# Optimization experiments

Measured on AMD Instinct MI355X. Metric: run time of the kernel, lower is better.

## Reference

```python
import jax, jax.numpy as jnp
import numpy as np

B, S, D, H, DFF, K = 16, 1024, 1024, 16, 4096, 3


def setup_inputs() -> dict:
    key = jax.random.key(0)
    ks = jax.random.split(key, 8)
    f = lambda k, sh: jax.random.normal(k, sh, jnp.float32) * 0.02
    return dict(
        x=jax.random.normal(ks[0], (B, S, D), jnp.float32),
        mask=jnp.ones((B, 1, S), jnp.int32),
        alpha1=jnp.ones((D,), jnp.float32), bias1=jnp.zeros((D,), jnp.float32),
        alpha2=jnp.ones((D,), jnp.float32), bias2=jnp.zeros((D,), jnp.float32),
        W_l1=f(ks[1], (D, 2 * D)), b_l1=jnp.zeros((2 * D,), jnp.float32),
        conv_w=f(ks[2], (H, K)),
        W_l2=f(ks[3], (D, D)), b_l2=jnp.zeros((D,), jnp.float32),
        W_ff1=f(ks[4], (D, DFF)), b_ff1=jnp.zeros((DFF,), jnp.float32),
        W_ff2=f(ks[5], (DFF, D)), b_ff2=jnp.zeros((D,), jnp.float32),
    )


def _norm(x, alpha, bias, eps=1e-6):
    # Norm: alpha * (x - mean) / (std + eps) + bias, torch std is unbiased (ddof=1)
    mu = x.mean(-1, keepdims=True)
    sd = x.std(-1, keepdims=True, ddof=1)
    return alpha * (x - mu) / (sd + eps) + bias


def _lightconv(x, conv_w):
    # x: [B, S, C]; conv_w: [H, K] softmax-normalized over K; channels in a head share kernel
    C = x.shape[-1]
    w = jax.nn.softmax(conv_w, axis=-1)              # [H, K]
    wk = jnp.repeat(w, C // H, axis=0)[:, None, :]   # [C, 1, K] depthwise kernel
    y = jax.lax.conv_general_dilated(
        x.transpose(0, 2, 1), wk, (1,), [(K // 2, (K - 1) // 2)],
        dimension_numbers=('NCH', 'OIH', 'NCH'), feature_group_count=C)
    return y.transpose(0, 2, 1)


def reference(x, mask, alpha1, bias1, alpha2, bias2, W_l1, b_l1, conv_w,
              W_l2, b_l2, W_ff1, b_ff1, W_ff2, b_ff2):
    # --- lightweight-conv sublayer ---
    res = x
    h = _norm(x, alpha1, bias1)
    h = h @ W_l1 + b_l1                         # [B,S,2C]
    a, b = jnp.split(h, 2, axis=-1)
    h = a * jax.nn.sigmoid(b)                   # GLU -> [B,S,C]
    cm = mask[:, -1, :][:, :, None]             # [B,S,1]
    h = jnp.where(cm == 0, 0.0, h)
    h = _lightconv(h, conv_w)
    h = h @ W_l2 + b_l2
    x = res + h
    # --- FFN sublayer ---
    res = x
    h = _norm(x, alpha2, bias2)
    h = jax.nn.relu(h @ W_ff1 + b_ff1) @ W_ff2 + b_ff2
    return res + h
```

## Files before the change

### kernel.cpp

```cpp
#include <hip/hip_runtime.h>

typedef unsigned short ushort_t;
typedef __attribute__((ext_vector_type(8))) short s8v;
typedef __attribute__((ext_vector_type(4))) float f4v;

__device__ __forceinline__ float b2f(ushort_t h) {
    union { unsigned u; float f; } c; c.u = ((unsigned)h) << 16; return c.f;
}
__device__ __forceinline__ ushort_t f2b(float f) {
    union { float f; unsigned u; } c; c.f = f;
    unsigned u = c.u;
    return (ushort_t)((u + 0x7fffu + ((u >> 16) & 1u)) >> 16);
}

__device__ __forceinline__ void glds16(const void* g, void* l) {
    __builtin_amdgcn_global_load_lds(
        (const __attribute__((address_space(1))) void*)g,
        (__attribute__((address_space(3))) void*)l, 16, 0, 0);
}

__global__ __launch_bounds__(256) void trans_k(const float* __restrict__ W,
                                               ushort_t* __restrict__ Wt,
                                               int K, int N) {
    __shared__ float tile[64][65];
    int k0 = blockIdx.x * 64, n0 = blockIdx.y * 64;
    int t = threadIdx.x;
    int c = t & 63, r4 = t >> 6;
#pragma unroll
    for (int i = 0; i < 16; ++i) {
        int r = i * 4 + r4;
        tile[r][c] = W[(size_t)(k0 + r) * N + n0 + c];
    }
    __syncthreads();
#pragma unroll
    for (int i = 0; i < 16; ++i) {
        int r = i * 4 + r4;
        Wt[(size_t)(n0 + r) * K + k0 + c] = f2b(tile[c][r]);
    }
}

__global__ __launch_bounds__(256) void norm_k(const float* __restrict__ x,
                                              const float* __restrict__ al,
                                              const float* __restrict__ be,
                                              ushort_t* __restrict__ out) {
    int row = blockIdx.x;
    const float4* xr = (const float4*)(x + (size_t)row * 1024);
    float4 v = xr[threadIdx.x];
    float s = v.x + v.y + v.z + v.w;
    float q = v.x * v.x + v.y * v.y + v.z * v.z + v.w * v.w;
#pragma unroll
    for (int o = 32; o > 0; o >>= 1) {
        s += __shfl_down(s, o);
        q += __shfl_down(q, o);
    }
    __shared__ float ss[4], qq[4];
    int lane = threadIdx.x & 63, wv = threadIdx.x >> 6;
    if (lane == 0) { ss[wv] = s; qq[wv] = q; }
    __syncthreads();
    s = ss[0] + ss[1] + ss[2] + ss[3];
    q = qq[0] + qq[1] + qq[2] + qq[3];
    float mu = s * (1.f / 1024.f);
    float var = (q - 1024.f * mu * mu) * (1.f / 1023.f);
    var = fmaxf(var, 0.f);
    float inv = 1.f / (sqrtf(var) + 1e-6f);
    float4 a4 = ((const float4*)al)[threadIdx.x];
    float4 b4 = ((const float4*)be)[threadIdx.x];
    ushort4 o4;
    o4.x = f2b(a4.x * (v.x - mu) * inv + b4.x);
    o4.y = f2b(a4.y * (v.y - mu) * inv + b4.y);
    o4.z = f2b(a4.z * (v.z - mu) * inv + b4.z);
    o4.w = f2b(a4.w * (v.w - mu) * inv + b4.w);
    ((ushort4*)(out + (size_t)row * 1024))[threadIdx.x] = o4;
}

__global__ __launch_bounds__(256) void glu_k(const ushort_t* __restrict__ t1,
                                             const int* __restrict__ mask,
                                             ushort_t* __restrict__ g) {
    int i = blockIdx.x * 256 + threadIdx.x;
    int row = i >> 7;
    int cc = (i & 127) << 3;
    int b = row >> 10, s = row & 1023;
    size_t base = (size_t)row * 2048;
    s8v va = *(const s8v*)(t1 + base + cc);
    s8v vb = *(const s8v*)(t1 + base + 1024 + cc);
    float mval = (mask[b * 1024 + s] == 0) ? 0.f : 1.f;
    s8v ov;
#pragma unroll
    for (int j = 0; j < 8; ++j) {
        float a = b2f((ushort_t)va[j]);
        float xx = b2f((ushort_t)vb[j]);
        float sg = 1.f / (1.f + __expf(-xx));
        ov[j] = (short)f2b(a * sg * mval);
    }
    *(s8v*)(g + (size_t)row * 1024 + cc) = ov;
}

__global__ __launch_bounds__(256) void conv_k(const ushort_t* __restrict__ g,
                                              const float* __restrict__ cw,
                                              ushort_t* __restrict__ out) {
    int i = blockIdx.x * 256 + threadIdx.x;
    int row = i >> 7;
    int cc = (i & 127) << 3;
    int s = row & 1023;
    int head = cc >> 6;
    float w0 = cw[head * 3 + 0], w1 = cw[head * 3 + 1], w2 = cw[head * 3 + 2];
    float mx = fmaxf(w0, fmaxf(w1, w2));
    float e0 = __expf(w0 - mx), e1 = __expf(w1 - mx), e2 = __expf(w2 - mx);
    float inv = 1.f / (e0 + e1 + e2);
    w0 = e0 * inv; w1 = e1 * inv; w2 = e2 * inv;
    size_t base = (size_t)row * 1024 + cc;
    s8v z = {0, 0, 0, 0, 0, 0, 0, 0};
    s8v vm = (s > 0)    ? *(const s8v*)(g + base - 1024) : z;
    s8v v0 = *(const s8v*)(g + base);
    s8v vp = (s < 1023) ? *(const s8v*)(g + base + 1024) : z;
    s8v ov;
#pragma unroll
    for (int j = 0; j < 8; ++j) {
        float r = w0 * b2f((ushort_t)vm[j]) + w1 * b2f((ushort_t)v0[j]) +
                  w2 * b2f((ushort_t)vp[j]);
        ov[j] = (short)f2b(r);
    }
    *(s8v*)(out + base) = ov;
}

template <int EPI>
__global__ __launch_bounds__(512, 1) void gemm_k(const ushort_t* __restrict__ A,
                                                 const ushort_t* __restrict__ Bt,
                                                 const float* __restrict__ bias,
                                                 const float* res, float* outf,
                                                 ushort_t* outb, int N, int K) {
    __shared__ char smem[131072] __attribute__((aligned(128)));
    const int NBN = N >> 8;
    const int nwg = gridDim.x;
    const int per = nwg >> 3;
    const int tt = (blockIdx.x & 7) * per + (blockIdx.x >> 3);
    const int gw = NBN << 3;
    const int g = tt / gw;
    const int rem = tt - g * gw;
    const int bm = (g << 3) + (rem & 7);
    const int bn = rem >> 3;

    const int t = threadIdx.x;
    const int l = t & 63, w = t >> 6;
    const int wm = w >> 2, wn = w & 3;
    const int lr = l & 15, lk = l >> 4;

    const int swzel = (((t & 3) ^ ((t >> 3) & 3)) << 3);
    const int r0 = t >> 2;
    const ushort_t* pA0 = A + (size_t)(bm * 256 + r0) * K + swzel;
    const ushort_t* pA1 = pA0 + (size_t)128 * K;
    const ushort_t* pB0 = Bt + (size_t)(bn * 256 + r0) * K + swzel;
    const ushort_t* pB1 = pB0 + (size_t)128 * K;

    const int fswz = ((lk ^ ((lr >> 1) & 3)) << 4);
    int aoff[8], boff[4];
#pragma unroll
    for (int m = 0; m < 8; ++m)
        aoff[m] = (wm * 128 + m * 16 + lr) * 64 + fswz;
#pragma unroll
    for (int n = 0; n < 4; ++n)
        boff[n] = 16384 + (wn * 64 + n * 16 + lr) * 64 + fswz;

    f4v acc[8][4];
#pragma unroll
    for (int m = 0; m < 8; ++m)
#pragma unroll
        for (int n = 0; n < 4; ++n) acc[m][n] = f4v{0.f, 0.f, 0.f, 0.f};

    const int NK = K >> 5;

#pragma unroll
    for (int p = 0; p < 3; ++p) {
        char* d = smem + p * 32768 + t * 16;
        glds16(pA0 + p * 32, d);
        glds16(pA1 + p * 32, d + 8192);
        glds16(pB0 + p * 32, d + 16384);
        glds16(pB1 + p * 32, d + 24576);
    }
    asm volatile("s_waitcnt vmcnt(8)");
    __builtin_amdgcn_s_barrier();
    __builtin_amdgcn_sched_barrier(0);

    s8v aL0[4], bF0[4], aL1[4], bF1[4], aH[4];
#pragma unroll
    for (int m = 0; m < 4; ++m) aL0[m] = *(const s8v*)(smem + aoff[m]);
#pragma unroll
    for (int n = 0; n < 4; ++n) bF0[n] = *(const s8v*)(smem + boff[n]);

#define KSTEP(I, CAL, CBF, NAL, NBF)                                           \
    {                                                                          \
        const int i_ = (I);                                                    \
        const char* cb_ = smem + (size_t)(i_ & 3) * 32768;                     \
        const char* nb_ = smem + (size_t)((i_ + 1) & 3) * 32768;               \
        int st_ = i_ + 3; if (st_ >= NK) st_ = NK - 1;                         \
        char* sd_ = smem + (size_t)((i_ + 3) & 3) * 32768 + t * 16;            \
        const int ko_ = st_ * 32;                                              \
                 \
        _Pragma("unroll")                                                      \
        for (int m = 0; m < 4; ++m) aH[m] = *(const s8v*)(cb_ + aoff[4 + m]);  \
        glds16(pA0 + ko_, sd_);                                                \
        glds16(pA1 + ko_, sd_ + 8192);                                         \
        glds16(pB0 + ko_, sd_ + 16384);                                        \
        glds16(pB1 + ko_, sd_ + 24576);                                        \
        __builtin_amdgcn_s_setprio(1);                                         \
        _Pragma("unroll")                                                      \
        for (int m = 0; m < 4; ++m)                                            \
            _Pragma("unroll")                                                  \
            for (int n = 0; n < 4; ++n)                                        \
                acc[m][n] = __builtin_amdgcn_mfma_f32_16x16x32_bf16(           \
                    CAL[m], CBF[n], acc[m][n], 0, 0, 0);                       \
        __builtin_amdgcn_s_setprio(0);                                         \
        __builtin_amdgcn_sched_barrier(0);                                     \
        asm volatile("s_waitcnt vmcnt(6)");               \
        __builtin_amdgcn_s_barrier();                                          \
        __builtin_amdgcn_sched_barrier(0);                                     \
           \
        _Pragma("unroll")                                                      \
        for (int m = 0; m < 4; ++m) NAL[m] = *(const s8v*)(nb_ + aoff[m]);     \
        _Pragma("unroll")                                                      \
        for (int n = 0; n < 4; ++n) NBF[n] = *(const s8v*)(nb_ + boff[n]);     \
        __builtin_amdgcn_s_setprio(1);                                         \
        _Pragma("unroll")                                                      \
        for (int m = 0; m < 4; ++m)                                            \
            _Pragma("unroll")                                                  \
            for (int n = 0; n < 4; ++n)                                        \
                acc[4 + m][n] = __builtin_amdgcn_mfma_f32_16x16x32_bf16(       \
                    aH[m], CBF[n], acc[4 + m][n], 0, 0, 0);                    \
        __builtin_amdgcn_s_setprio(0);                                         \
    }

    for (int ii = 0; ii < NK; ii += 2) {
        KSTEP(ii, aL0, bF0, aL1, bF1);
        KSTEP(ii + 1, aL1, bF1, aL0, bF0);
    }
#undef KSTEP

    if (EPI == 1) {
#pragma unroll
        for (int n = 0; n < 4; ++n) {
            int gcol = bn * 256 + wn * 64 + n * 16 + lr;
            float bb = bias[gcol];
#pragma unroll
            for (int m = 0; m < 8; ++m) {
#pragma unroll
                for (int r = 0; r < 4; ++r) {
                    int grow = bm * 256 + wm * 128 + m * 16 + lk * 4 + r;
                    size_t oi = (size_t)grow * N + gcol;
                    outf[oi] = acc[m][n][r] + bb + res[oi];
                }
            }
        }
    } else {
        asm volatile("s_waitcnt vmcnt(0)" ::: "memory");
        __builtin_amdgcn_s_barrier();
        float bb4[4];
#pragma unroll
        for (int n = 0; n < 4; ++n)
            bb4[n] = bias[bn * 256 + wn * 64 + n * 16 + lr];
#pragma unroll
        for (int m = 0; m < 8; ++m)
#pragma unroll
            for (int n = 0; n < 4; ++n)
#pragma unroll
                for (int r = 0; r < 4; ++r) {
                    int row = wm * 128 + m * 16 + lk * 4 + r;
                    int colb = ((wn * 64 + n * 16 + lr) * 2) ^ ((row & 3) << 4);
                    float v = acc[m][n][r] + bb4[n];
                    if (EPI == 2) v = fmaxf(v, 0.f);
                    *(ushort_t*)(smem + row * 512 + colb) = f2b(v);
                }
        __builtin_amdgcn_s_barrier();
#pragma unroll
        for (int s = 0; s < 16; ++s) {
            int row = s * 16 + (t >> 5);
            int byt = row * 512 + (((t & 31) * 16) ^ ((row & 3) << 4));
            int grow = bm * 256 + row;
            int gcol = bn * 256 + (t & 31) * 8;
            *(s8v*)(outb + (size_t)grow * N + gcol) = *(const s8v*)(smem + byt);
        }
    }
}

extern "C" void kernel_launch(void* const* d_in, const int* in_sizes, int n_in,
                              void* d_out, int out_size, void* d_ws, size_t ws_size,
                              hipStream_t stream) {
    const float* x      = (const float*)d_in[0];
    const int*   mask   = (const int*)d_in[1];
    const float* alpha1 = (const float*)d_in[2];
    const float* bias1  = (const float*)d_in[3];
    const float* alpha2 = (const float*)d_in[4];
    const float* bias2  = (const float*)d_in[5];
    const float* W_l1   = (const float*)d_in[6];
    const float* b_l1   = (const float*)d_in[7];
    const float* conv_w = (const float*)d_in[8];
    const float* W_l2   = (const float*)d_in[9];
    const float* b_l2   = (const float*)d_in[10];
    const float* W_ff1  = (const float*)d_in[11];
    const float* b_ff1  = (const float*)d_in[12];
    const float* W_ff2  = (const float*)d_in[13];
    const float* b_ff2  = (const float*)d_in[14];
    float* out = (float*)d_out;

    char* ws = (char*)d_ws;
    size_t off = 0;
    auto alloc = [&](size_t b) {
        char* p = ws + off;
        off += (b + 255) & ~(size_t)255;
        return p;
    };
    ushort_t* Wl1t  = (ushort_t*)alloc(2048ull * 1024 * 2);
    ushort_t* Wl2t  = (ushort_t*)alloc(1024ull * 1024 * 2);
    ushort_t* Wff1t = (ushort_t*)alloc(4096ull * 1024 * 2);
    ushort_t* Wff2t = (ushort_t*)alloc(1024ull * 4096 * 2);
    char* regA = alloc(134217728ull);
    ushort_t* B1 = (ushort_t*)alloc(33554432ull);
    ushort_t* C1 = (ushort_t*)alloc(33554432ull);
    ushort_t* t1 = (ushort_t*)regA;
    ushort_t* f1 = (ushort_t*)regA;

    const int R = 16384;

    trans_k<<<dim3(16, 32), 256, 0, stream>>>(W_l1, Wl1t, 1024, 2048);
    trans_k<<<dim3(16, 16), 256, 0, stream>>>(W_l2, Wl2t, 1024, 1024);
    trans_k<<<dim3(16, 64), 256, 0, stream>>>(W_ff1, Wff1t, 1024, 4096);
    trans_k<<<dim3(64, 16), 256, 0, stream>>>(W_ff2, Wff2t, 4096, 1024);

    norm_k<<<R, 256, 0, stream>>>(x, alpha1, bias1, B1);
    gemm_k<0><<<64 * 8, 512, 0, stream>>>(B1, Wl1t, b_l1, nullptr, nullptr, t1, 2048, 1024);
    glu_k<<<8192, 256, 0, stream>>>(t1, mask, B1);
    conv_k<<<8192, 256, 0, stream>>>(B1, conv_w, C1);
    gemm_k<1><<<64 * 4, 512, 0, stream>>>(C1, Wl2t, b_l2, x, out, nullptr, 1024, 1024);

    norm_k<<<R, 256, 0, stream>>>(out, alpha2, bias2, B1);
    gemm_k<2><<<64 * 16, 512, 0, stream>>>(B1, Wff1t, b_ff1, nullptr, nullptr, f1, 4096, 1024);
    gemm_k<1><<<64 * 4, 512, 0, stream>>>(f1, Wff2t, b_ff2, out, out, nullptr, 1024, 4096);
}
```

Baseline: 585.2 us.

## Fuse GLU into conv kernel and switch GEMM to double-buffered 64-wide K steps

```diff
diff --git a/kernel.cpp b/kernel.cpp
--- a/kernel.cpp
+++ b/kernel.cpp
@@ -73,54 +73,41 @@
     ((ushort4*)(out + (size_t)row * 1024))[threadIdx.x] = o4;
 }
 
-__global__ __launch_bounds__(256) void glu_k(const ushort_t* __restrict__ t1,
-                                             const int* __restrict__ mask,
-                                             ushort_t* __restrict__ g) {
+__global__ __launch_bounds__(256) void gluconv_k(const ushort_t* __restrict__ t1,
+                                                 const int* __restrict__ mask,
+                                                 const float* __restrict__ cw,
+                                                 ushort_t* __restrict__ out) {
     int i = blockIdx.x * 256 + threadIdx.x;
     int row = i >> 7;
     int cc = (i & 127) << 3;
     int b = row >> 10, s = row & 1023;
-    size_t base = (size_t)row * 2048;
-    s8v va = *(const s8v*)(t1 + base + cc);
-    s8v vb = *(const s8v*)(t1 + base + 1024 + cc);
-    float mval = (mask[b * 1024 + s] == 0) ? 0.f : 1.f;
-    s8v ov;
-#pragma unroll
-    for (int j = 0; j < 8; ++j) {
-        float a = b2f((ushort_t)va[j]);
-        float xx = b2f((ushort_t)vb[j]);
-        float sg = 1.f / (1.f + __expf(-xx));
-        ov[j] = (short)f2b(a * sg * mval);
-    }
-    *(s8v*)(g + (size_t)row * 1024 + cc) = ov;
-}
-
-__global__ __launch_bounds__(256) void conv_k(const ushort_t* __restrict__ g,
-                                              const float* __restrict__ cw,
-                                              ushort_t* __restrict__ out) {
-    int i = blockIdx.x * 256 + threadIdx.x;
-    int row = i >> 7;
-    int cc = (i & 127) << 3;
-    int s = row & 1023;
     int head = cc >> 6;
     float w0 = cw[head * 3 + 0], w1 = cw[head * 3 + 1], w2 = cw[head * 3 + 2];
     float mx = fmaxf(w0, fmaxf(w1, w2));
     float e0 = __expf(w0 - mx), e1 = __expf(w1 - mx), e2 = __expf(w2 - mx);
     float inv = 1.f / (e0 + e1 + e2);
-    w0 = e0 * inv; w1 = e1 * inv; w2 = e2 * inv;
-    size_t base = (size_t)row * 1024 + cc;
-    s8v z = {0, 0, 0, 0, 0, 0, 0, 0};
-    s8v vm = (s > 0)    ? *(const s8v*)(g + base - 1024) : z;
-    s8v v0 = *(const s8v*)(g + base);
-    s8v vp = (s < 1023) ? *(const s8v*)(g + base + 1024) : z;
+    float wt[3] = {e0 * inv, e1 * inv, e2 * inv};
+    float a8[8] = {0.f, 0.f, 0.f, 0.f, 0.f, 0.f, 0.f, 0.f};
+#pragma unroll
+    for (int tap = 0; tap < 3; ++tap) {
+        int ss = s + tap - 1;
+        if (ss < 0 || ss > 1023) continue;
+        float wm = (mask[b * 1024 + ss] == 0) ? 0.f : wt[tap];
+        size_t base = (size_t)(row + tap - 1) * 2048 + cc;
+        s8v va = *(const s8v*)(t1 + base);
+        s8v vb = *(const s8v*)(t1 + base + 1024);
+#pragma unroll
+        for (int j = 0; j < 8; ++j) {
+            float a = b2f((ushort_t)va[j]);
+            float xx = b2f((ushort_t)vb[j]);
+            float sg = 1.f / (1.f + __expf(-xx));
+            a8[j] += wm * a * sg;
+        }
+    }
     s8v ov;
 #pragma unroll
-    for (int j = 0; j < 8; ++j) {
-        float r = w0 * b2f((ushort_t)vm[j]) + w1 * b2f((ushort_t)v0[j]) +
-                  w2 * b2f((ushort_t)vp[j]);
-        ov[j] = (short)f2b(r);
-    }
-    *(s8v*)(out + base) = ov;
+    for (int j = 0; j < 8; ++j) ov[j] = (short)f2b(a8[j]);
+    *(s8v*)(out + (size_t)row * 1024 + cc) = ov;
 }
 
 template <int EPI>
@@ -159,7 +146,7 @@
         aoff[m] = (wm * 128 + m * 16 + lr) * 64 + fswz;
 #pragma unroll
     for (int n = 0; n < 4; ++n)
-        boff[n] = 16384 + (wn * 64 + n * 16 + lr) * 64 + fswz;
+        boff[n] = 32768 + (wn * 64 + n * 16 + lr) * 64 + fswz;
 
     f4v acc[8][4];
 #pragma unroll
@@ -167,71 +154,100 @@
 #pragma unroll
         for (int n = 0; n < 4; ++n) acc[m][n] = f4v{0.f, 0.f, 0.f, 0.f};
 
-    const int NK = K >> 5;
-
-#pragma unroll
-    for (int p = 0; p < 3; ++p) {
-        char* d = smem + p * 32768 + t * 16;
-        glds16(pA0 + p * 32, d);
-        glds16(pA1 + p * 32, d + 8192);
-        glds16(pB0 + p * 32, d + 16384);
-        glds16(pB1 + p * 32, d + 24576);
-    }
-    asm volatile("s_waitcnt vmcnt(8)");
+    const int NK = K >> 6;
+
+    glds16(pA0 + 0, smem + t * 16);
+    glds16(pA1 + 0, smem + 8192 + t * 16);
+    glds16(pA0 + 32, smem + 16384 + t * 16);
+    glds16(pA1 + 32, smem + 24576 + t * 16);
+    glds16(pB0 + 0, smem + 32768 + t * 16);
+    glds16(pB1 + 0, smem + 40960 + t * 16);
+    glds16(pB0 + 32, smem + 49152 + t * 16);
+    glds16(pB1 + 32, smem + 57344 + t * 16);
+    asm volatile("s_waitcnt vmcnt(0)");
     __builtin_amdgcn_s_barrier();
     __builtin_amdgcn_sched_barrier(0);
 
-    s8v aL0[4], bF0[4], aL1[4], bF1[4], aH[4];
-#pragma unroll
-    for (int m = 0; m < 4; ++m) aL0[m] = *(const s8v*)(smem + aoff[m]);
-#pragma unroll
-    for (int n = 0; n < 4; ++n) bF0[n] = *(const s8v*)(smem + boff[n]);
-
-#define KSTEP(I, CAL, CBF, NAL, NBF)                                           \
+    s8v a0[4], b0[4], a1[4], b1[4];
+#pragma unroll
+    for (int m = 0; m < 4; ++m) a0[m] = *(const s8v*)(smem + aoff[m]);
+#pragma unroll
+    for (int n = 0; n < 4; ++n) b0[n] = *(const s8v*)(smem + boff[n]);
+
+#define KSTEP(I, CA, CB, NA, NB)                                               \
     {                                                                          \
         const int i_ = (I);                                                    \
-        const char* cb_ = smem + (size_t)(i_ & 3) * 32768;                     \
-        const char* nb_ = smem + (size_t)((i_ + 1) & 3) * 32768;               \
-        int st_ = i_ + 3; if (st_ >= NK) st_ = NK - 1;                         \
-        char* sd_ = smem + (size_t)((i_ + 3) & 3) * 32768 + t * 16;            \
-        const int ko_ = st_ * 32;                                              \
-                 \
-        _Pragma("unroll")                                                      \
-        for (int m = 0; m < 4; ++m) aH[m] = *(const s8v*)(cb_ + aoff[4 + m]);  \
-        glds16(pA0 + ko_, sd_);                                                \
-        glds16(pA1 + ko_, sd_ + 8192);                                         \
-        glds16(pB0 + ko_, sd_ + 16384);                                        \
-        glds16(pB1 + ko_, sd_ + 24576);                                        \
+        const char* cb_ = smem + (size_t)(i_ & 1) * 65536;                     \
+        const char* nb_ = smem + (size_t)((i_ + 1) & 1) * 65536;               \
+        char* sb_ = smem + (size_t)((i_ + 1) & 1) * 65536 + t * 16;            \
+        const int nx_ = (i_ + 1 < NK ? i_ + 1 : NK - 1) * 64;                  \
+            \
+        glds16(pA0 + nx_, sb_);                                                \
+        glds16(pA1 + nx_, sb_ + 8192);                                         \
+        glds16(pA0 + nx_ + 32, sb_ + 16384);                                   \
+        glds16(pA1 + nx_ + 32, sb_ + 24576);                                   \
+        glds16(pB0 + nx_, sb_ + 32768);                                        \
+        glds16(pB1 + nx_, sb_ + 40960);                                        \
+        glds16(pB0 + nx_ + 32, sb_ + 49152);                                   \
+        glds16(pB1 + nx_ + 32, sb_ + 57344);                                   \
+        s8v aH0[4], aL1[4], bK1[4], aH1[4];                                    \
+        _Pragma("unroll")                                                      \
+        for (int m = 0; m < 4; ++m) aH0[m] = *(const s8v*)(cb_ + aoff[4 + m]); \
         __builtin_amdgcn_s_setprio(1);                                         \
         _Pragma("unroll")                                                      \
         for (int m = 0; m < 4; ++m)                                            \
             _Pragma("unroll")                                                  \
             for (int n = 0; n < 4; ++n)                                        \
                 acc[m][n] = __builtin_amdgcn_mfma_f32_16x16x32_bf16(           \
-                    CAL[m], CBF[n], acc[m][n], 0, 0, 0);                       \
+                    CA[m], CB[n], acc[m][n], 0, 0, 0);                         \
         __builtin_amdgcn_s_setprio(0);                                         \
-        __builtin_amdgcn_sched_barrier(0);                                     \
-        asm volatile("s_waitcnt vmcnt(6)");               \
-        __builtin_amdgcn_s_barrier();                                          \
-        __builtin_amdgcn_sched_barrier(0);                                     \
-           \
-        _Pragma("unroll")                                                      \
-        for (int m = 0; m < 4; ++m) NAL[m] = *(const s8v*)(nb_ + aoff[m]);     \
-        _Pragma("unroll")                                                      \
-        for (int n = 0; n < 4; ++n) NBF[n] = *(const s8v*)(nb_ + boff[n]);     \
+        _Pragma("unroll")                                                      \
+        for (int m = 0; m < 4; ++m)                                            \
+            aL1[m] = *(const s8v*)(cb_ + 16384 + aoff[m]);                     \
+        _Pragma("unroll")                                                      \
+        for (int n = 0; n < 4; ++n)                                            \
+            bK1[n] = *(const s8v*)(cb_ + 16384 + boff[n]);                     \
         __builtin_amdgcn_s_setprio(1);                                         \
         _Pragma("unroll")                                                      \
         for (int m = 0; m < 4; ++m)                                            \
             _Pragma("unroll")                                                  \
             for (int n = 0; n < 4; ++n)                                        \
                 acc[4 + m][n] = __builtin_amdgcn_mfma_f32_16x16x32_bf16(       \
-                    aH[m], CBF[n], acc[4 + m][n], 0, 0, 0);                    \
+                    aH0[m], CB[n], acc[4 + m][n], 0, 0, 0);                    \
         __builtin_amdgcn_s_setprio(0);                                         \
+        _Pragma("unroll")                                                      \
+        for (int m = 0; m < 4; ++m)                                            \
+            aH1[m] = *(const s8v*)(cb_ + 16384 + aoff[4 + m]);                 \
+        __builtin_amdgcn_s_setprio(1);                                         \
+        _Pragma("unroll")                                                      \
+        for (int m = 0; m < 4; ++m)                                            \
+            _Pragma("unroll")                                                  \
+            for (int n = 0; n < 4; ++n)                                        \
+                acc[m][n] = __builtin_amdgcn_mfma_f32_16x16x32_bf16(           \
+                    aL1[m], bK1[n], acc[m][n], 0, 0, 0);                       \
+        __builtin_amdgcn_s_setprio(0);                                         \
+        __builtin_amdgcn_sched_barrier(0);                                     \
+        asm volatile("s_waitcnt vmcnt(0)");    \
+        __builtin_amdgcn_sched_barrier(0);                                     \
+        __builtin_amdgcn_s_barrier();                                          \
+        __builtin_amdgcn_sched_barrier(0);                                     \
+        _Pragma("unroll")                                                      \
+        for (int m = 0; m < 4; ++m) NA[m] = *(const s8v*)(nb_ + aoff[m]);      \
+        _Pragma("unroll")                                                      \
+        for (int n = 0; n < 4; ++n) NB[n] = *(const s8v*)(nb_ + boff[n]);      \
+        __builtin_amdgcn_s_setprio(1);                                         \
+        _Pragma("unroll")                                                      \
+        for (int m = 0; m < 4; ++m)                                            \
+            _Pragma("unroll")                                                  \
+            for (int n = 0; n < 4; ++n)                                        \
+                acc[4 + m][n] = __builtin_amdgcn_mfma_f32_16x16x32_bf16(       \
+                    aH1[m], bK1[n], acc[4 + m][n], 0, 0, 0);                   \
+        __builtin_amdgcn_s_setprio(0);                                         \
     }
 
     for (int ii = 0; ii < NK; ii += 2) {
-        KSTEP(ii, aL0, bF0, aL1, bF1);
-        KSTEP(ii + 1, aL1, bF1, aL0, bF0);
+        KSTEP(ii, a0, b0, a1, b1);
+        KSTEP(ii + 1, a1, b1, a0, b0);
     }
 #undef KSTEP
 
@@ -251,7 +267,7 @@
             }
         }
     } else {
-        asm volatile("s_waitcnt vmcnt(0)" ::: "memory");
+        asm volatile("s_waitcnt vmcnt(0)");
         __builtin_amdgcn_s_barrier();
         float bb4[4];
 #pragma unroll
@@ -327,8 +343,7 @@
 
     norm_k<<<R, 256, 0, stream>>>(x, alpha1, bias1, B1);
     gemm_k<0><<<64 * 8, 512, 0, stream>>>(B1, Wl1t, b_l1, nullptr, nullptr, t1, 2048, 1024);
-    glu_k<<<8192, 256, 0, stream>>>(t1, mask, B1);
-    conv_k<<<8192, 256, 0, stream>>>(B1, conv_w, C1);
+    gluconv_k<<<8192, 256, 0, stream>>>(t1, mask, conv_w, C1);
     gemm_k<1><<<64 * 4, 512, 0, stream>>>(C1, Wl2t, b_l2, x, out, nullptr, 1024, 1024);
 
     norm_k<<<R, 256, 0, stream>>>(out, alpha2, bias2, B1);
```

Measured after the change: 602.2 us. 2.9% more time.

## Fuse GLU and mask into first GEMM epilogue via interleaved weight columns

Applied to the files above, without the earlier changes.

```diff
diff --git a/kernel.cpp b/kernel.cpp
--- a/kernel.cpp
+++ b/kernel.cpp
@@ -19,6 +19,7 @@
         (__attribute__((address_space(3))) void*)l, 16, 0, 0);
 }
 
+template <int PERM>
 __global__ __launch_bounds__(256) void trans_k(const float* __restrict__ W,
                                                ushort_t* __restrict__ Wt,
                                                int K, int N) {
@@ -35,7 +36,16 @@
 #pragma unroll
     for (int i = 0; i < 16; ++i) {
         int r = i * 4 + r4;
-        Wt[(size_t)(n0 + r) * K + k0 + c] = f2b(tile[c][r]);
+        int s = n0 + r;
+        int d;
+        if (PERM) {
+            int a = (s < 1024);
+            int s2 = a ? s : s - 1024;
+            d = ((s2 >> 7) << 8) + (a ? 0 : 128) + (s2 & 127);
+        } else {
+            d = s;
+        }
+        Wt[(size_t)d * K + k0 + c] = f2b(tile[c][r]);
     }
 }
 
@@ -71,28 +81,6 @@
     o4.z = f2b(a4.z * (v.z - mu) * inv + b4.z);
     o4.w = f2b(a4.w * (v.w - mu) * inv + b4.w);
     ((ushort4*)(out + (size_t)row * 1024))[threadIdx.x] = o4;
-}
-
-__global__ __launch_bounds__(256) void glu_k(const ushort_t* __restrict__ t1,
-                                             const int* __restrict__ mask,
-                                             ushort_t* __restrict__ g) {
-    int i = blockIdx.x * 256 + threadIdx.x;
-    int row = i >> 7;
-    int cc = (i & 127) << 3;
-    int b = row >> 10, s = row & 1023;
-    size_t base = (size_t)row * 2048;
-    s8v va = *(const s8v*)(t1 + base + cc);
-    s8v vb = *(const s8v*)(t1 + base + 1024 + cc);
-    float mval = (mask[b * 1024 + s] == 0) ? 0.f : 1.f;
-    s8v ov;
-#pragma unroll
-    for (int j = 0; j < 8; ++j) {
-        float a = b2f((ushort_t)va[j]);
-        float xx = b2f((ushort_t)vb[j]);
-        float sg = 1.f / (1.f + __expf(-xx));
-        ov[j] = (short)f2b(a * sg * mval);
-    }
-    *(s8v*)(g + (size_t)row * 1024 + cc) = ov;
 }
 
 __global__ __launch_bounds__(256) void conv_k(const ushort_t* __restrict__ g,
@@ -127,6 +115,7 @@
 __global__ __launch_bounds__(512, 1) void gemm_k(const ushort_t* __restrict__ A,
                                                  const ushort_t* __restrict__ Bt,
                                                  const float* __restrict__ bias,
+                                                 const int* __restrict__ maskp,
                                                  const float* res, float* outf,
                                                  ushort_t* outb, int N, int K) {
     __shared__ char smem[131072] __attribute__((aligned(128)));
@@ -255,8 +244,13 @@
         __builtin_amdgcn_s_barrier();
         float bb4[4];
 #pragma unroll
-        for (int n = 0; n < 4; ++n)
-            bb4[n] = bias[bn * 256 + wn * 64 + n * 16 + lr];
+        for (int n = 0; n < 4; ++n) {
+            int d = bn * 256 + wn * 64 + n * 16 + lr;
+            int src = d;
+            if (EPI == 3)
+                src = ((d >> 8) << 7) + (d & 127) + (((d >> 7) & 1) << 10);
+            bb4[n] = bias[src];
+        }
 #pragma unroll
         for (int m = 0; m < 8; ++m)
 #pragma unroll
@@ -270,13 +264,36 @@
                     *(ushort_t*)(smem + row * 512 + colb) = f2b(v);
                 }
         __builtin_amdgcn_s_barrier();
-#pragma unroll
-        for (int s = 0; s < 16; ++s) {
-            int row = s * 16 + (t >> 5);
-            int byt = row * 512 + (((t & 31) * 16) ^ ((row & 3) << 4));
-            int grow = bm * 256 + row;
-            int gcol = bn * 256 + (t & 31) * 8;
-            *(s8v*)(outb + (size_t)grow * N + gcol) = *(const s8v*)(smem + byt);
+        if (EPI == 3) {
+#pragma unroll
+            for (int s = 0; s < 8; ++s) {
+                int row = s * 32 + (t >> 4);
+                int abyt = row * 512 + (((t & 15) * 16) ^ ((row & 3) << 4));
+                s8v av = *(const s8v*)(smem + abyt);
+                s8v bv = *(const s8v*)(smem + abyt + 256);
+                int grow = bm * 256 + row;
+                float mval =
+                    (maskp[(grow >> 10) * 1024 + (grow & 1023)] == 0) ? 0.f : 1.f;
+                s8v ov;
+#pragma unroll
+                for (int j = 0; j < 8; ++j) {
+                    float a = b2f((ushort_t)av[j]);
+                    float xx = b2f((ushort_t)bv[j]);
+                    ov[j] = (short)f2b(a * mval / (1.f + __expf(-xx)));
+                }
+                *(s8v*)(outb + (size_t)grow * (N >> 1) + bn * 128 +
+                        (t & 15) * 8) = ov;
+            }
+        } else {
+#pragma unroll
+            for (int s = 0; s < 16; ++s) {
+                int row = s * 16 + (t >> 5);
+                int byt = row * 512 + (((t & 31) * 16) ^ ((row & 3) << 4));
+                int grow = bm * 256 + row;
+                int gcol = bn * 256 + (t & 31) * 8;
+                *(s8v*)(outb + (size_t)grow * N + gcol) =
+                    *(const s8v*)(smem + byt);
+            }
         }
     }
 }
@@ -315,23 +332,26 @@
     char* regA = alloc(134217728ull);
     ushort_t* B1 = (ushort_t*)alloc(33554432ull);
     ushort_t* C1 = (ushort_t*)alloc(33554432ull);
-    ushort_t* t1 = (ushort_t*)regA;
+    ushort_t* G1 = (ushort_t*)regA;
     ushort_t* f1 = (ushort_t*)regA;
 
     const int R = 16384;
 
-    trans_k<<<dim3(16, 32), 256, 0, stream>>>(W_l1, Wl1t, 1024, 2048);
-    trans_k<<<dim3(16, 16), 256, 0, stream>>>(W_l2, Wl2t, 1024, 1024);
-    trans_k<<<dim3(16, 64), 256, 0, stream>>>(W_ff1, Wff1t, 1024, 4096);
-    trans_k<<<dim3(64, 16), 256, 0, stream>>>(W_ff2, Wff2t, 4096, 1024);
+    trans_k<1><<<dim3(16, 32), 256, 0, stream>>>(W_l1, Wl1t, 1024, 2048);
+    trans_k<0><<<dim3(16, 16), 256, 0, stream>>>(W_l2, Wl2t, 1024, 1024);
+    trans_k<0><<<dim3(16, 64), 256, 0, stream>>>(W_ff1, Wff1t, 1024, 4096);
+    trans_k<0><<<dim3(64, 16), 256, 0, stream>>>(W_ff2, Wff2t, 4096, 1024);
 
     norm_k<<<R, 256, 0, stream>>>(x, alpha1, bias1, B1);
-    gemm_k<0><<<64 * 8, 512, 0, stream>>>(B1, Wl1t, b_l1, nullptr, nullptr, t1, 2048, 1024);
-    glu_k<<<8192, 256, 0, stream>>>(t1, mask, B1);
-    conv_k<<<8192, 256, 0, stream>>>(B1, conv_w, C1);
-    gemm_k<1><<<64 * 4, 512, 0, stream>>>(C1, Wl2t, b_l2, x, out, nullptr, 1024, 1024);
+    gemm_k<3><<<64 * 8, 512, 0, stream>>>(B1, Wl1t, b_l1, mask, nullptr,
+                                          nullptr, G1, 2048, 1024);
+    conv_k<<<8192, 256, 0, stream>>>(G1, conv_w, C1);
+    gemm_k<1><<<64 * 4, 512, 0, stream>>>(C1, Wl2t, b_l2, nullptr, x, out,
+                                          nullptr, 1024, 1024);
 
     norm_k<<<R, 256, 0, stream>>>(out, alpha2, bias2, B1);
-    gemm_k<2><<<64 * 16, 512, 0, stream>>>(B1, Wff1t, b_ff1, nullptr, nullptr, f1, 4096, 1024);
-    gemm_k<1><<<64 * 4, 512, 0, stream>>>(f1, Wff2t, b_ff2, out, out, nullptr, 1024, 4096);
-}
+    gemm_k<2><<<64 * 16, 512, 0, stream>>>(B1, Wff1t, b_ff1, nullptr, nullptr,
+                                           nullptr, f1, 4096, 1024);
+    gemm_k<1><<<64 * 4, 512, 0, stream>>>(f1, Wff2t, b_ff2, nullptr, out, out,
+                                          nullptr, 1024, 4096);
+}
```

Measured after the change: 549.0 us. 6.2% less time.
